# Kernel optimization log

Measured on AMD Instinct MI355X. Metric: run time of the kernel, lower is better.

The kernel has to match this reference:

```python
import jax, jax.numpy as jnp
import numpy as np

B, S, D = 4, 2048, 2048


def setup_inputs() -> dict:
    key = jax.random.key(0)
    ks = jax.random.split(key, 24)
    sc = 1.0 / np.sqrt(D)
    def lin(ki, kb):
        W = jax.random.normal(ks[ki], (D, D), dtype=jnp.float32) * sc
        b = jax.random.normal(ks[kb], (D,), dtype=jnp.float32) * 0.01
        return W, b
    Wi, bWi = lin(0, 1); Ui, bUi = lin(2, 3)
    Wf, bWf = lin(4, 5); Uf, bUf = lin(6, 7)
    Wc, bWc = lin(8, 9); Uc, bUc = lin(10, 11)
    Wo, bWo = lin(12, 13); Uo, bUo = lin(14, 15)
    Wp, bp = lin(16, 17)
    x = jax.random.normal(ks[18], (B, S, D), dtype=jnp.float32)
    h = jax.random.normal(ks[19], (B, S, D), dtype=jnp.float32)
    return dict(x=x, h=h, Wi=Wi, bWi=bWi, Ui=Ui, bUi=bUi,
                Wf=Wf, bWf=bWf, Uf=Uf, bUf=bUf,
                Wc=Wc, bWc=bWc, Uc=Uc, bUc=bUc,
                Wo=Wo, bWo=bWo, Uo=Uo, bUo=bUo,
                Wp=Wp, bp=bp)


def reference(x, h, Wi, bWi, Ui, bUi, Wf, bWf, Uf, bUf,
              Wc, bWc, Uc, bUc, Wo, bWo, Uo, bUo, Wp, bp):
    # In the torch source, h[:, t, :] is read BEFORE being overwritten at step t,
    # and c is zero-initialized with each slot written once (so f * c_prev == 0).
    # Hence the computation is exactly parallel over the time axis.
    Zi = jnp.einsum('bsd,ed->bse', x, Wi) + bWi + jnp.einsum('bsd,ed->bse', h, Ui) + bUi
    Zf = jnp.einsum('bsd,ed->bse', x, Wf) + bWf + jnp.einsum('bsd,ed->bse', h, Uf) + bUf
    Zc = jnp.einsum('bsd,ed->bse', x, Wc) + bWc + jnp.einsum('bsd,ed->bse', h, Uc) + bUc
    Zo = jnp.einsum('bsd,ed->bse', x, Wo) + bWo + jnp.einsum('bsd,ed->bse', h, Uo) + bUo
    i = jnp.exp(Zi)
    f = jnp.exp(Zf)  # multiplies a zero cell state in the source; kept for fidelity
    c = f * jnp.zeros_like(f) + i * jnp.tanh(Zc)
    h_out = jax.nn.sigmoid(Zo) * jnp.tanh(c)
    hidden_state = h_out[:, -1, :] @ Wp.T + bp
    return (hidden_state, c)
```

## Files before the change

### kernel.cpp

```cpp
#include <hip/hip_runtime.h>
#include <hip/hip_bf16.h>

typedef short short8 __attribute__((ext_vector_type(8)));
typedef unsigned short ushort8v __attribute__((ext_vector_type(8)));
typedef float f32x4 __attribute__((ext_vector_type(4)));

#define D_DIM 2048
#define KTOT 4096
#define M_TOT 8192
#define NPACK 4096


__device__ __forceinline__ unsigned short f2bf(float f) {
    union { float f; unsigned u; } c; c.f = f;
    unsigned u = c.u;
    u += 0x7fffu + ((u >> 16) & 1u);
    return (unsigned short)(u >> 16);
}

__device__ __forceinline__ float fast_tanh(float x) {
    float ax = fabsf(x);
    float ez = __expf(2.0f * fminf(ax, 15.0f));
    float t = (ez - 1.0f) / (ez + 1.0f);
    return copysignf(t, x);
}

#define GLOAD_LDS16(g, l)                                                     \
    __builtin_amdgcn_global_load_lds(                                         \
        (const __attribute__((address_space(1))) void*)(g),                   \
        (__attribute__((address_space(3))) void*)(l), 16, 0, 0)

#define WAITVM_(N) asm volatile("s_waitcnt vmcnt(" #N ")" ::: "memory")
#define WAITVM(N)  WAITVM_(N)
#define WAITLG_(N) asm volatile("s_waitcnt lgkmcnt(" #N ")" ::: "memory")
#define WAITLG(N)  WAITLG_(N)


__global__ __launch_bounds__(256)
void pack2(const float* __restrict__ X, const float* __restrict__ H,
           __hip_bfloat16* __restrict__ dst, int total8) {
    int t = blockIdx.x * 256 + threadIdx.x;
    if (t >= total8) return;
    long e0 = (long)t * 8;
    long r  = e0 >> 12;
    int  k  = (int)(e0 & 4095);
    const float* src = (k < D_DIM) ? (X + r * D_DIM + k)
                                   : (H + r * D_DIM + (k - D_DIM));
    float4 v0 = *(const float4*)(src);
    float4 v1 = *(const float4*)(src + 4);
    ushort8v o;
    o[0] = f2bf(v0.x); o[1] = f2bf(v0.y); o[2] = f2bf(v0.z); o[3] = f2bf(v0.w);
    o[4] = f2bf(v1.x); o[5] = f2bf(v1.y); o[6] = f2bf(v1.z); o[7] = f2bf(v1.w);
    *(ushort8v*)(dst + e0) = o;
}


__global__ __launch_bounds__(256)
void pack_gates(const float* __restrict__ Wi, const float* __restrict__ Ui,
                const float* __restrict__ Wc, const float* __restrict__ Uc,
                __hip_bfloat16* __restrict__ dst) {
    int t = blockIdx.x * 256 + threadIdx.x;
    const int g = t >> 9;
    const int k = (t & 511) * 8;
    const int w = g & 31;
    const int n = ((g >> 5) << 4) | (w & 15);
    const float* Wm = (w & 16) ? Wc : Wi;
    const float* Um = (w & 16) ? Uc : Ui;
    const float* src = (k < D_DIM) ? (Wm + (size_t)n * D_DIM + k)
                                   : (Um + (size_t)n * D_DIM + (k - D_DIM));
    float4 v0 = *(const float4*)(src);
    float4 v1 = *(const float4*)(src + 4);
    ushort8v o;
    o[0] = f2bf(v0.x); o[1] = f2bf(v0.y); o[2] = f2bf(v0.z); o[3] = f2bf(v0.w);
    o[4] = f2bf(v1.x); o[5] = f2bf(v1.y); o[6] = f2bf(v1.z); o[7] = f2bf(v1.w);
    *(ushort8v*)(dst + (size_t)g * KTOT + k) = o;
}


#define BK 64
#define NT (KTOT / BK)

__device__ __forceinline__ void mfma16(f32x4 (&acc)[8][4], int mb,
                                       const short8 (&a)[4], const short8 (&b)[4]) {
    #pragma unroll
    for (int m = 0; m < 4; ++m)
        #pragma unroll
        for (int n = 0; n < 4; ++n)
            acc[mb + m][n] = __builtin_amdgcn_mfma_f32_16x16x32_bf16(
                a[m], b[n], acc[mb + m][n], 0, 0, 0);
}

#define READ4(dst, base, IMM)                                                 \
    { _Pragma("unroll")                                                       \
      for (int m_ = 0; m_ < 4; ++m_)                                          \
          dst[m_] = *(const short8*)((base) + (IMM) + m_ * 1024); }

#define STAGE_A(DIMM, KB)                                                     \
    { GLOAD_LDS16(gA0 + (KB), ldsA + (DIMM) + dOff);                          \
      GLOAD_LDS16(gA1 + (KB), ldsA + (DIMM) + dOff + 1024); }
#define STAGE_B(DIMM, KB)                                                     \
    { GLOAD_LDS16(gB0 + (KB), ldsB + (DIMM) + dOff);                          \
      GLOAD_LDS16(gB1 + (KB), ldsB + (DIMM) + dOff + 1024); }

#define TILE(CUR, NXT, V1, V3, ST12, ST34, PF4)                               \
  {                                                                           \
                    \
    READ4(aQ, rdA, (CUR) + 4096);                                             \
    if (ST12) STAGE_A((NXT) + 16384, kb + 64);                                \
    WAITVM(V1);                                                               \
    __builtin_amdgcn_s_barrier();                                             \
    WAITLG(4);                                                                \
    __builtin_amdgcn_sched_barrier(0);                                        \
    __builtin_amdgcn_s_setprio(1); mfma16(acc, 0, aP, bP);                    \
    __builtin_amdgcn_s_setprio(0);                                            \
           \
    READ4(aP, rdA, (CUR) + 16384);                                            \
    READ4(bQ, rdB, (CUR) + 16384);                                            \
    if (ST12) STAGE_B((NXT) + 16384, kb + 64);                                \
    __builtin_amdgcn_s_barrier();                                             \
    WAITLG(8);                                                                \
    __builtin_amdgcn_sched_barrier(0);                                        \
    __builtin_amdgcn_s_setprio(1); mfma16(acc, 4, aQ, bP);                    \
    __builtin_amdgcn_s_setprio(0);                                            \
                    \
    READ4(aQ, rdA, (CUR) + 16384 + 4096);                                     \
    if (ST34) STAGE_A((CUR), kb + 128);                                       \
    WAITVM(V3);                                                               \
    __builtin_amdgcn_s_barrier();                                             \
    WAITLG(4);                                                                \
    __builtin_amdgcn_sched_barrier(0);                                        \
    __builtin_amdgcn_s_setprio(1); mfma16(acc, 0, aP, bQ);                    \
    __builtin_amdgcn_s_setprio(0);                                            \
      \
    if (PF4) { READ4(aP, rdA, (NXT)); READ4(bP, rdB, (NXT)); }                \
    if (ST34) STAGE_B((CUR), kb + 128);                                       \
    __builtin_amdgcn_s_barrier();                                             \
    if (PF4) { WAITLG(8); } else { WAITLG(0); }                               \
    __builtin_amdgcn_sched_barrier(0);                                        \
    __builtin_amdgcn_s_setprio(1); mfma16(acc, 4, aQ, bQ);                    \
    __builtin_amdgcn_s_setprio(0);                                            \
  }

__global__ __launch_bounds__(512, 2)
void gemm8(const __hip_bfloat16* __restrict__ A,
           const __hip_bfloat16* __restrict__ Bp,
           const float* __restrict__ bWi, const float* __restrict__ bUi,
           const float* __restrict__ bWc, const float* __restrict__ bUc,
           float* __restrict__ Cout) {
    __shared__ __hip_bfloat16 sA[2][2][256][32];
    __shared__ __hip_bfloat16 sB[2][2][256][32];

    const int tid  = threadIdx.x;
    const int wid  = tid >> 6;
    const int lane = tid & 63;

    int bid = blockIdx.x;
    bid = (bid & 7) * 64 + (bid >> 3);
    const int tn = (bid & 15) * 256;
    const int tm = (bid >> 4) * 256;

    const int wr  = (wid >> 2) * 128;
    const int wc  = (wid & 3) * 64;
    const int r15 = lane & 15;
    const int uswz16 = (((lane >> 4) ^ ((r15 >> 1) & 3)) * 16);

    const int Lb0  = wid * 128 + lane;
    const int row0 = Lb0 >> 2;
    const int u0   = (Lb0 & 3) ^ ((Lb0 >> 3) & 3);
    const char* gA0 = (const char*)(A  + (size_t)(tm + row0) * KTOT) + u0 * 16;
    const char* gA1 = gA0 + (size_t)16 * KTOT * 2;
    const char* gB0 = (const char*)(Bp + (size_t)(tn + row0) * KTOT) + u0 * 16;
    const char* gB1 = gB0 + (size_t)16 * KTOT * 2;
    char* ldsA = (char*)sA;
    char* ldsB = (char*)sB;
    const int dOff = Lb0 * 16;

    const char* rdA = (const char*)sA + (wr + r15) * 64 + uswz16;
    const char* rdB = (const char*)sB + (wc + r15) * 64 + uswz16;

    f32x4 acc[8][4] = {};
    short8 aP[4], aQ[4], bP[4], bQ[4];

    STAGE_A(0, 0);        STAGE_B(0, 0);
    STAGE_A(16384, 64);   STAGE_B(16384, 64);
    STAGE_A(32768, 128);  STAGE_B(32768, 128);
    WAITVM(8);
    __builtin_amdgcn_s_barrier();
    READ4(aP, rdA, 0);
    READ4(bP, rdB, 0);

    int kb = 128;
    #pragma unroll 1
    for (int it = 0; it < 31; ++it) {
        TILE(0, 32768, 6, 6, 1, 1, 1); kb += 128;
        TILE(32768, 0, 6, 6, 1, 1, 1); kb += 128;
    }
    TILE(0, 32768, 6, 4, 1, 0, 1); kb += 128;
    TILE(32768, 0, 0, 0, 0, 0, 0);

    const int rg4 = (lane >> 4) * 4;
    #pragma unroll
    for (int q = 0; q < 2; ++q) {
        const int gn = (tn >> 1) + (wc >> 1) + q * 16 + r15;
        const float bi_ = bWi[gn] + bUi[gn];
        const float bc_ = bWc[gn] + bUc[gn];
        #pragma unroll
        for (int m = 0; m < 8; ++m) {
            const int gm = tm + wr + m * 16 + rg4;
            #pragma unroll
            for (int r = 0; r < 4; ++r) {
                const float zi = acc[m][2 * q][r]     + bi_;
                const float zc = acc[m][2 * q + 1][r] + bc_;
                Cout[(size_t)(gm + r) * D_DIM + gn] = __expf(zi) * fast_tanh(zc);
            }
        }
    }
}


__global__ __launch_bounds__(256)
void last_gate(const float* __restrict__ x, const float* __restrict__ h,
               const float* __restrict__ Wo, const float* __restrict__ bWo,
               const float* __restrict__ Uo, const float* __restrict__ bUo,
               const float* __restrict__ cfull, float* __restrict__ hbuf) {
    const int o    = blockIdx.x * 4 + (threadIdx.x >> 6);
    const int lane = threadIdx.x & 63;
    const int b = o >> 11, e = o & 2047;
    const float* xr = x  + ((size_t)b * D_DIM + (D_DIM - 1)) * D_DIM;
    const float* hr = h  + ((size_t)b * D_DIM + (D_DIM - 1)) * D_DIM;
    const float* wo = Wo + (size_t)e * D_DIM;
    const float* uo = Uo + (size_t)e * D_DIM;
    float s = 0.0f;
    for (int d = lane; d < D_DIM; d += 64)
        s += xr[d] * wo[d] + hr[d] * uo[d];
    #pragma unroll
    for (int off = 32; off; off >>= 1) s += __shfl_down(s, off);
    if (lane == 0) {
        const float zo  = s + bWo[e] + bUo[e];
        const float sig = 1.0f / (1.0f + __expf(-zo));
        const float cv  = cfull[((size_t)b * D_DIM + (D_DIM - 1)) * D_DIM + e];
        hbuf[o] = sig * fast_tanh(cv);
    }
}


__global__ __launch_bounds__(256)
void proj(const float* __restrict__ hbuf, const float* __restrict__ Wp,
          const float* __restrict__ bp, float* __restrict__ out) {
    const int o    = blockIdx.x * 4 + (threadIdx.x >> 6);
    const int lane = threadIdx.x & 63;
    const int b = o >> 11, p = o & 2047;
    const float* hv = hbuf + (size_t)b * D_DIM;
    const float* wp = Wp   + (size_t)p * D_DIM;
    float s = 0.0f;
    for (int e = lane; e < D_DIM; e += 64)
        s += hv[e] * wp[e];
    #pragma unroll
    for (int off = 32; off; off >>= 1) s += __shfl_down(s, off);
    if (lane == 0) out[o] = s + bp[p];
}


extern "C" void kernel_launch(void* const* d_in, const int* in_sizes, int n_in,
                              void* d_out, int out_size, void* d_ws, size_t ws_size,
                              hipStream_t stream) {
    const float* x   = (const float*)d_in[0];
    const float* h   = (const float*)d_in[1];
    const float* Wi  = (const float*)d_in[2];  const float* bWi = (const float*)d_in[3];
    const float* Ui  = (const float*)d_in[4];  const float* bUi = (const float*)d_in[5];
    const float* Wc  = (const float*)d_in[10]; const float* bWc = (const float*)d_in[11];
    const float* Uc  = (const float*)d_in[12]; const float* bUc = (const float*)d_in[13];
    const float* Wo  = (const float*)d_in[14]; const float* bWo = (const float*)d_in[15];
    const float* Uo  = (const float*)d_in[16]; const float* bUo = (const float*)d_in[17];
    const float* Wp  = (const float*)d_in[18]; const float* bp  = (const float*)d_in[19];

    float* out = (float*)d_out;
    char*  ws  = (char*)d_ws;

    __hip_bfloat16* Abf  = (__hip_bfloat16*)ws;
    __hip_bfloat16* Bpk  = (__hip_bfloat16*)(ws + ((size_t)64 << 20));
    float*          hbuf = (float*)(ws + ((size_t)96 << 20));

    pack2<<<16384, 256, 0, stream>>>(x, h, Abf, M_TOT * KTOT / 8);
    pack_gates<<<8192, 256, 0, stream>>>(Wi, Ui, Wc, Uc, Bpk);

    gemm8<<<(M_TOT / 256) * (NPACK / 256), 512, 0, stream>>>(
        Abf, Bpk, bWi, bUi, bWc, bUc, out + 8192);

    last_gate<<<2048, 256, 0, stream>>>(x, h, Wo, bWo, Uo, bUo, out + 8192,
                                        (float*)hbuf);
    proj<<<2048, 256, 0, stream>>>(hbuf, Wp, bp, out);
}
```

Measured before the change: 333.2 us.

## Restructure GEMM main loop to BK=64 K-tiles with new LDS layout and staging

Reorganizes the bf16 MFMA GEMM inner loop: shared tiles become 128x64 halves with a new XOR swizzle, and each K-tile step loads two k-subblocks per fragment and issues paired MFMAs. The staging schedule changes so A and B halves are prefetched in a staggered pattern across four sub-phases, each wrapped in barriers with full lgkmcnt waits. This aims to cut the number of LDS read and wait points per K step and to improve global-load coalescing. In exchange it adds extra barriers and stricter waits, which could serialise the LDS reads with the MFMA work.

Measured after the change: 320.0 us. 4.0% less time.

```diff
diff --git a/kernel.cpp b/kernel.cpp
--- a/kernel.cpp
+++ b/kernel.cpp
@@ -32,8 +32,11 @@
 
 #define WAITVM_(N) asm volatile("s_waitcnt vmcnt(" #N ")" ::: "memory")
 #define WAITVM(N)  WAITVM_(N)
-#define WAITLG_(N) asm volatile("s_waitcnt lgkmcnt(" #N ")" ::: "memory")
-#define WAITLG(N)  WAITLG_(N)
+#define WAITLG0    asm volatile("s_waitcnt lgkmcnt(0)" ::: "memory")
+#define BAR        __builtin_amdgcn_s_barrier()
+#define SCHB       __builtin_amdgcn_sched_barrier(0)
+#define PRIO1      __builtin_amdgcn_s_setprio(1)
+#define PRIO0      __builtin_amdgcn_s_setprio(0)
 
 
 __global__ __launch_bounds__(256)
@@ -77,69 +80,59 @@
 }
 
 
-#define BK 64
-#define NT (KTOT / BK)
-
-__device__ __forceinline__ void mfma16(f32x4 (&acc)[8][4], int mb,
-                                       const short8 (&a)[4], const short8 (&b)[4]) {
-    #pragma unroll
-    for (int m = 0; m < 4; ++m)
-        #pragma unroll
-        for (int n = 0; n < 4; ++n)
-            acc[mb + m][n] = __builtin_amdgcn_mfma_f32_16x16x32_bf16(
-                a[m], b[n], acc[mb + m][n], 0, 0, 0);
-}
-
-#define READ4(dst, base, IMM)                                                 \
-    { _Pragma("unroll")                                                       \
-      for (int m_ = 0; m_ < 4; ++m_)                                          \
-          dst[m_] = *(const short8*)((base) + (IMM) + m_ * 1024); }
-
-#define STAGE_A(DIMM, KB)                                                     \
-    { GLOAD_LDS16(gA0 + (KB), ldsA + (DIMM) + dOff);                          \
-      GLOAD_LDS16(gA1 + (KB), ldsA + (DIMM) + dOff + 1024); }
-#define STAGE_B(DIMM, KB)                                                     \
-    { GLOAD_LDS16(gB0 + (KB), ldsB + (DIMM) + dOff);                          \
-      GLOAD_LDS16(gB1 + (KB), ldsB + (DIMM) + dOff + 1024); }
-
-#define TILE(CUR, NXT, V1, V3, ST12, ST34, PF4)                               \
-  {                                                                           \
-                    \
-    READ4(aQ, rdA, (CUR) + 4096);                                             \
-    if (ST12) STAGE_A((NXT) + 16384, kb + 64);                                \
-    WAITVM(V1);                                                               \
-    __builtin_amdgcn_s_barrier();                                             \
-    WAITLG(4);                                                                \
-    __builtin_amdgcn_sched_barrier(0);                                        \
-    __builtin_amdgcn_s_setprio(1); mfma16(acc, 0, aP, bP);                    \
-    __builtin_amdgcn_s_setprio(0);                                            \
-           \
-    READ4(aP, rdA, (CUR) + 16384);                                            \
-    READ4(bQ, rdB, (CUR) + 16384);                                            \
-    if (ST12) STAGE_B((NXT) + 16384, kb + 64);                                \
-    __builtin_amdgcn_s_barrier();                                             \
-    WAITLG(8);                                                                \
-    __builtin_amdgcn_sched_barrier(0);                                        \
-    __builtin_amdgcn_s_setprio(1); mfma16(acc, 4, aQ, bP);                    \
-    __builtin_amdgcn_s_setprio(0);                                            \
-                    \
-    READ4(aQ, rdA, (CUR) + 16384 + 4096);                                     \
-    if (ST34) STAGE_A((CUR), kb + 128);                                       \
-    WAITVM(V3);                                                               \
-    __builtin_amdgcn_s_barrier();                                             \
-    WAITLG(4);                                                                \
-    __builtin_amdgcn_sched_barrier(0);                                        \
-    __builtin_amdgcn_s_setprio(1); mfma16(acc, 0, aP, bQ);                    \
-    __builtin_amdgcn_s_setprio(0);                                            \
-      \
-    if (PF4) { READ4(aP, rdA, (NXT)); READ4(bP, rdB, (NXT)); }                \
-    if (ST34) STAGE_B((CUR), kb + 128);                                       \
-    __builtin_amdgcn_s_barrier();                                             \
-    if (PF4) { WAITLG(8); } else { WAITLG(0); }                               \
-    __builtin_amdgcn_sched_barrier(0);                                        \
-    __builtin_amdgcn_s_setprio(1); mfma16(acc, 4, aQ, bQ);                    \
-    __builtin_amdgcn_s_setprio(0);                                            \
+__device__ __forceinline__ f32x4 mf(short8 a, short8 b, f32x4 c) {
+    return __builtin_amdgcn_mfma_f32_16x16x32_bf16(a, b, c, 0, 0, 0);
+}
+
+#define RD4A(BUF, IMM)                                                        \
+  { _Pragma("unroll") for (int m_ = 0; m_ < 4; ++m_) {                        \
+      ak0[m_] = *(const short8*)(rdA0 + (BUF) + (IMM) + m_ * 2048);           \
+      ak1[m_] = *(const short8*)(rdA1 + (BUF) + (IMM) + m_ * 2048); } }
+
+#define RDB(d0, d1, BUF, IMM)                                                 \
+  { _Pragma("unroll") for (int n_ = 0; n_ < 2; ++n_) {                        \
+      d0[n_] = *(const short8*)(rdB0 + (BUF) + (IMM) + n_ * 2048);            \
+      d1[n_] = *(const short8*)(rdB1 + (BUF) + (IMM) + n_ * 2048); } }
+
+#define MF16(MB, NB, bk0, bk1)                                                \
+  { _Pragma("unroll") for (int m_ = 0; m_ < 4; ++m_)                          \
+    _Pragma("unroll") for (int n_ = 0; n_ < 2; ++n_) {                        \
+      acc[(MB)+m_][(NB)+n_] = mf(ak0[m_], bk0[n_], acc[(MB)+m_][(NB)+n_]);    \
+      acc[(MB)+m_][(NB)+n_] = mf(ak1[m_], bk1[n_], acc[(MB)+m_][(NB)+n_]); } }
+
+#define SA0(BUFB, KB) { GLOAD_LDS16(gAh0 + (KB), ldsA + (BUFB) + dOff);       \
+                        GLOAD_LDS16(gAh0 + (KB) + 524288, ldsA + (BUFB) + dOff + 8192); }
+#define SA1(BUFB, KB) { GLOAD_LDS16(gAh1 + (KB), ldsA + (BUFB) + 16384 + dOff); \
+                        GLOAD_LDS16(gAh1 + (KB) + 524288, ldsA + (BUFB) + 16384 + dOff + 8192); }
+#define SB0(BUFB, KB) { GLOAD_LDS16(gBh0 + (KB), ldsB + (BUFB) + dOff);       \
+                        GLOAD_LDS16(gBh0 + (KB) + 524288, ldsB + (BUFB) + dOff + 8192); }
+#define SB1(BUFB, KB) { GLOAD_LDS16(gBh1 + (KB), ldsB + (BUFB) + 16384 + dOff); \
+                        GLOAD_LDS16(gBh1 + (KB) + 524288, ldsB + (BUFB) + 16384 + dOff + 8192); }
+
+#define KTILE(BUF, S1, S2, S3, S4, VMN)                                       \
+  {           \
+    RD4A(BUF, 0);                                                             \
+    RDB(b01k0, b01k1, BUF, 0);                                                \
+    S1;                                                                       \
+    BAR; WAITLG0; SCHB;                                                       \
+    PRIO1; MF16(0, 0, b01k0, b01k1); PRIO0; BAR;                              \
+                                 \
+    RDB(b23k0, b23k1, BUF, 4096);                                             \
+    S2;                                                                       \
+    BAR; WAITLG0; SCHB;                                                       \
+    PRIO1; MF16(0, 2, b23k0, b23k1); PRIO0; BAR;                              \
+                                 \
+    RD4A(BUF, 8192);                                                          \
+    S3;                                                                       \
+    BAR; WAITLG0; SCHB;                                                       \
+    PRIO1; MF16(4, 0, b01k0, b01k1); PRIO0; BAR;                              \
+                          \
+    S4; VMN;                                                                  \
+    BAR; SCHB;                                                                \
+    PRIO1; MF16(4, 2, b23k0, b23k1); PRIO0; BAR;                              \
   }
+
+#define NOSTG (void)0
 
 __global__ __launch_bounds__(512, 2)
 void gemm8(const __hip_bfloat16* __restrict__ A,
@@ -147,8 +140,8 @@
            const float* __restrict__ bWi, const float* __restrict__ bUi,
            const float* __restrict__ bWc, const float* __restrict__ bUc,
            float* __restrict__ Cout) {
-    __shared__ __hip_bfloat16 sA[2][2][256][32];
-    __shared__ __hip_bfloat16 sB[2][2][256][32];
+    __shared__ __hip_bfloat16 sA[2][2][128][64];
+    __shared__ __hip_bfloat16 sB[2][2][128][64];
 
     const int tid  = threadIdx.x;
     const int wid  = tid >> 6;
@@ -162,41 +155,53 @@
     const int wr  = (wid >> 2) * 128;
     const int wc  = (wid & 3) * 64;
     const int r15 = lane & 15;
-    const int uswz16 = (((lane >> 4) ^ ((r15 >> 1) & 3)) * 16);
-
-    const int Lb0  = wid * 128 + lane;
-    const int row0 = Lb0 >> 2;
-    const int u0   = (Lb0 & 3) ^ ((Lb0 >> 3) & 3);
-    const char* gA0 = (const char*)(A  + (size_t)(tm + row0) * KTOT) + u0 * 16;
-    const char* gA1 = gA0 + (size_t)16 * KTOT * 2;
-    const char* gB0 = (const char*)(Bp + (size_t)(tn + row0) * KTOT) + u0 * 16;
-    const char* gB1 = gB0 + (size_t)16 * KTOT * 2;
+    const int g   = lane >> 4;
+
+    const int sb    = g ^ (r15 & 3);
+    const int khb   = (r15 >> 2) & 1;
+    const int slot0 = (khb * 4 + sb) * 16;
+    const int slot1 = (((1 ^ khb) * 4) + sb) * 16;
+
+    const char* rdA0 = (const char*)sA + (wr >> 7) * 16384 + r15 * 128 + slot0;
+    const char* rdA1 = (const char*)sA + (wr >> 7) * 16384 + r15 * 128 + slot1;
+    const char* rdB0 = (const char*)sB + (wc >> 7) * 16384 + (wc & 64) * 128 + r15 * 128 + slot0;
+    const char* rdB1 = (const char*)sB + (wc >> 7) * 16384 + (wc & 64) * 128 + r15 * 128 + slot1;
+
+    const int r0 = tid >> 3, s0 = tid & 7;
+    const int colb = (((s0 >> 2) ^ ((r0 >> 2) & 1)) * 64) +
+                     (((s0 & 3) ^ (r0 & 3)) * 16);
+    const char* gAh0 = (const char*)(A  + (size_t)(tm + r0) * KTOT) + colb;
+    const char* gAh1 = gAh0 + (size_t)128 * KTOT * 2;
+    const char* gBh0 = (const char*)(Bp + (size_t)(tn + r0) * KTOT) + colb;
+    const char* gBh1 = gBh0 + (size_t)128 * KTOT * 2;
     char* ldsA = (char*)sA;
     char* ldsB = (char*)sB;
-    const int dOff = Lb0 * 16;
-
-    const char* rdA = (const char*)sA + (wr + r15) * 64 + uswz16;
-    const char* rdB = (const char*)sB + (wc + r15) * 64 + uswz16;
+    const int dOff = tid * 16;
 
     f32x4 acc[8][4] = {};
-    short8 aP[4], aQ[4], bP[4], bQ[4];
-
-    STAGE_A(0, 0);        STAGE_B(0, 0);
-    STAGE_A(16384, 64);   STAGE_B(16384, 64);
-    STAGE_A(32768, 128);  STAGE_B(32768, 128);
-    WAITVM(8);
-    __builtin_amdgcn_s_barrier();
-    READ4(aP, rdA, 0);
-    READ4(bP, rdB, 0);
-
-    int kb = 128;
+    short8 ak0[4], ak1[4], b01k0[2], b01k1[2], b23k0[2], b23k1[2];
+
+    SB0(0, 0); SB1(0, 0); SA0(0, 0); SA1(0, 0);
+    SB0(32768, 128); SB1(32768, 128);
+    WAITVM(4);
+    BAR;
+
+    int kb = 0;
     #pragma unroll 1
-    for (int it = 0; it < 31; ++it) {
-        TILE(0, 32768, 6, 6, 1, 1, 1); kb += 128;
-        TILE(32768, 0, 6, 6, 1, 1, 1); kb += 128;
+    for (int i = 0; i < 31; ++i) {
+        KTILE(0,
+              SA0(32768, kb + 128), SA1(32768, kb + 128),
+              SB0(0, kb + 256),     SB1(0, kb + 256),
+              WAITVM(4));
+        KTILE(32768,
+              SA0(0, kb + 256),     SA1(0, kb + 256),
+              SB0(32768, kb + 384), SB1(32768, kb + 384),
+              WAITVM(4));
+        kb += 256;
     }
-    TILE(0, 32768, 6, 4, 1, 0, 1); kb += 128;
-    TILE(32768, 0, 0, 0, 0, 0, 0);
+    KTILE(0, SA0(32768, kb + 128), SA1(32768, kb + 128),
+          NOSTG, NOSTG, WAITVM(0));
+    KTILE(32768, NOSTG, NOSTG, NOSTG, NOSTG, NOSTG);
 
     const int rg4 = (lane >> 4) * 4;
     #pragma unroll
```
